# Kernel optimization log

Measured on AMD Instinct MI355X. Metric: run time of the kernel, lower is better.

The kernel has to match this reference:

```python
import jax, jax.numpy as jnp
import numpy as np

H = 16  # num_heads


def setup_inputs() -> dict:
    key = jax.random.key(0)
    ks = jax.random.split(key, 7)
    S, HID, D = 8192, 1280, 80
    n_chunks = 8
    x = jax.random.normal(ks[0], (S, HID), dtype=jnp.float32)
    cos = jax.random.uniform(ks[1], (S, D), dtype=jnp.float32)
    sin = jax.random.uniform(ks[2], (S, D), dtype=jnp.float32)
    Wqkv = jax.random.normal(ks[3], (HID, 3 * HID), dtype=jnp.float32) * (HID ** -0.5)
    bqkv = jnp.zeros((3 * HID,), dtype=jnp.float32)
    Wproj = jax.random.normal(ks[4], (HID, HID), dtype=jnp.float32) * (HID ** -0.5)
    bproj = jnp.zeros((HID,), dtype=jnp.float32)
    cu_seqlens = (jnp.arange(n_chunks + 1, dtype=jnp.int32) * (S // n_chunks))
    return {"x": x, "cos": cos, "sin": sin, "Wqkv": Wqkv, "bqkv": bqkv,
            "Wproj": Wproj, "bproj": bproj, "cu_seqlens": cu_seqlens}


def _apply_rotary(t, cos, sin):
    # t: (S, H, D); cos/sin: (S, D)
    d2 = t.shape[-1] // 2
    x1, x2 = t[..., :d2], t[..., d2:]
    rotated = jnp.concatenate([-x2, x1], axis=-1)
    return t * cos[:, None, :] + rotated * sin[:, None, :]


def reference(x, cos, sin, Wqkv, bqkv, Wproj, bproj, cu_seqlens):
    S, HID = x.shape
    D = HID // H
    inv_scale = 1.0 / np.sqrt(D)
    qkv = (x @ Wqkv + bqkv).reshape(S, 3, H, D)
    q, k, v = qkv[:, 0], qkv[:, 1], qkv[:, 2]  # each (S, H, D)
    q = _apply_rotary(q, cos, sin)
    k = _apply_rotary(k, cos, sin)
    # Equal-size windows: reshape to (n_chunks, L, H, D) -> block-diagonal attention.
    C = cu_seqlens.shape[0] - 1
    L = S // C
    qc = q.reshape(C, L, H, D)
    kc = k.reshape(C, L, H, D)
    vc = v.reshape(C, L, H, D)
    scores = jnp.einsum('cihd,cjhd->chij', qc, kc) * inv_scale
    probs = jax.nn.softmax(scores.astype(jnp.float32), axis=-1).astype(x.dtype)
    out = jnp.einsum('chij,cjhd->cihd', probs, vc)  # (C, L, H, D)
    out = out.reshape(S, HID)
    return out @ Wproj + bproj
```

## Files before the change

### kernel.cpp

```cpp
#include <hip/hip_runtime.h>
#include <math.h>
#include <stdint.h>

#define S_LEN 8192
#define HID   1280
#define NH    16
#define HD    80
#define LCH   1024
#define NCH   8

typedef __attribute__((ext_vector_type(8))) short bf16x8;
typedef __attribute__((ext_vector_type(4))) float f32x4;

__device__ __forceinline__ uint16_t f2bf(float f) {
    union { float f; uint32_t u; } v; v.f = f;
    uint32_t r = v.u + 0x7FFF + ((v.u >> 16) & 1);
    return (uint16_t)(r >> 16);
}
__device__ __forceinline__ float bf2f(uint16_t h) {
    union { uint32_t u; float f; } v; v.u = ((uint32_t)h) << 16;
    return v.f;
}
__device__ __forceinline__ uint16_t f2bf_trunc(float f) {
    union { float f; uint32_t u; } v; v.f = f;
    return (uint16_t)(v.u >> 16);
}

__device__ __forceinline__ void glds16(const void* g, void* l) {
    __builtin_amdgcn_global_load_lds(
        (const __attribute__((address_space(1))) uint32_t*)g,
        (__attribute__((address_space(3))) uint32_t*)l,
        16, 0, 0);
}

#define MFMA16(a, b, c) __builtin_amdgcn_mfma_f32_16x16x32_bf16(a, b, c, 0, 0, 0)
#define SB()  __builtin_amdgcn_sched_barrier(0)
#define BAR() __builtin_amdgcn_s_barrier()

template<int N> __device__ __forceinline__ void vmwait() {
    if constexpr (N == 0) asm volatile("s_waitcnt vmcnt(0)" ::: "memory");
    else if constexpr (N == 2) asm volatile("s_waitcnt vmcnt(2)" ::: "memory");
    else if constexpr (N == 3) asm volatile("s_waitcnt vmcnt(3)" ::: "memory");
    else if constexpr (N == 4) asm volatile("s_waitcnt vmcnt(4)" ::: "memory");
}

__device__ __forceinline__ void stage_tile(const char* gsrc, char* dst, int w,
                                           int kt, int nbytes)
{
    const char* sp = gsrc + (size_t)kt * 64;
    int off = w * 1024;
    glds16(sp + (size_t)off * 40, dst + off);
    off += 8192;
    if (off < nbytes) glds16(sp + (size_t)off * 40, dst + off);
}

__global__ __launch_bounds__(256)
void xsplit_kernel(const float* __restrict__ x, uint16_t* __restrict__ xh,
                   uint16_t* __restrict__ xl)
{
    int idx = (blockIdx.x * 256 + threadIdx.x) * 4;
    float4 v = *(const float4*)(x + idx);
    ushort4 hi, lo;
    hi.x = f2bf(v.x); lo.x = f2bf(v.x - bf2f(hi.x));
    hi.y = f2bf(v.y); lo.y = f2bf(v.y - bf2f(hi.y));
    hi.z = f2bf(v.z); lo.z = f2bf(v.z - bf2f(hi.z));
    hi.w = f2bf(v.w); lo.w = f2bf(v.w - bf2f(hi.w));
    *(ushort4*)(xh + idx) = hi;
    *(ushort4*)(xl + idx) = lo;
}

template<int ND>
__global__ __launch_bounds__(256)
void wsplit_kernel(const float* __restrict__ W, uint16_t* __restrict__ Wth,
                   uint16_t* __restrict__ Wtl)
{
    __shared__ float t[32][33];
    const int tid = threadIdx.x;
    const int n0 = blockIdx.x * 32;
    const int k0 = blockIdx.y * 32;
    for (int i = tid; i < 1024; i += 256) {
        int r = i >> 5, c = i & 31;
        t[r][c] = W[(size_t)(k0 + r) * ND + n0 + c];
    }
    __syncthreads();
    for (int i = tid; i < 1024; i += 256) {
        int r = i >> 5, c = i & 31;
        float f = t[c][r];
        uint16_t hi = f2bf(f);
        size_t o = (size_t)(n0 + r) * HID + k0 + c;
        Wth[o] = hi;
        Wtl[o] = f2bf(f - bf2f(hi));
    }
}

template<int ND, int BN, int NWN, int EPI, int W2, int W3>
__global__ __launch_bounds__(512, 2)
void gemm8p(const uint16_t* __restrict__ Ahp, const uint16_t* __restrict__ Alp,
            const uint16_t* __restrict__ Bth, const uint16_t* __restrict__ Btl,
            const float* __restrict__ bias, float* __restrict__ oF,
            uint16_t* __restrict__ oq, uint16_t* __restrict__ ok,
            uint16_t* __restrict__ ov)
{
    constexpr int NWM = 8 / NWN;
    constexpr int MI  = 256 / (NWM * 16);
    constexpr int NI  = BN / (NWN * 16);
    constexpr int ABYTES = 256 * 64;
    constexpr int BBYTES = BN * 64;
    constexpr int NT = HID / 32;
    static_assert(BN % (NWN * 16) == 0, "tile split");

    __shared__ __align__(1024) uint16_t AsH[2][ABYTES / 2];
    __shared__ __align__(1024) uint16_t AsL[2][ABYTES / 2];
    __shared__ __align__(1024) uint16_t BsH[2][BBYTES / 2];
    __shared__ __align__(1024) uint16_t BsL[2][BBYTES / 2];

    const int tid  = threadIdx.x;
    const int w    = tid >> 6;
    const int lane = tid & 63;
    const int quad = lane >> 4;
    const int l16  = lane & 15;
    const int wm   = w / NWN;
    const int wn   = w % NWN;

    const int n0 = blockIdx.x * BN;
    const int m0 = blockIdx.y * 256;

    const size_t stg = (size_t)(lane >> 2) * (HID * 2)
                     + (size_t)(((lane & 3) ^ ((lane >> 3) & 3)) << 4);
    const char* gAh = (const char*)Ahp + (size_t)m0 * (HID * 2) + stg;
    const char* gAl = (const char*)Alp + (size_t)m0 * (HID * 2) + stg;
    const char* gBh = (const char*)Bth + (size_t)n0 * (HID * 2) + stg;
    const char* gBl = (const char*)Btl + (size_t)n0 * (HID * 2) + stg;

    const int swz  = (quad ^ ((l16 >> 1) & 3)) << 4;
    const int aoff = (wm * (MI * 16) + l16) * 64 + swz;
    const int boff = (wn * (NI * 16) + l16) * 64 + swz;

    f32x4 acc[MI][NI];
    #pragma unroll
    for (int mi = 0; mi < MI; ++mi)
        #pragma unroll
        for (int ni = 0; ni < NI; ++ni) acc[mi][ni] = (f32x4){0.f, 0.f, 0.f, 0.f};

    stage_tile(gAh, (char*)AsH[0], w, 0, ABYTES);
    stage_tile(gBh, (char*)BsH[0], w, 0, BBYTES);
    stage_tile(gBl, (char*)BsL[0], w, 0, BBYTES);
    stage_tile(gAl, (char*)AsL[0], w, 0, ABYTES);
    SB(); vmwait<W3>(); BAR(); SB();

    for (int kt = 0; kt < NT - 1; ++kt) {
        const int s = kt & 1, t = s ^ 1;
        bf16x8 ah[MI], bh[NI];

        #pragma unroll
        for (int mi = 0; mi < MI; ++mi)
            ah[mi] = *(const bf16x8*)((const char*)AsH[s] + aoff + mi * 1024);
        #pragma unroll
        for (int ni = 0; ni < NI; ++ni)
            bh[ni] = *(const bf16x8*)((const char*)BsH[s] + boff + ni * 1024);
        stage_tile(gAh, (char*)AsH[t], w, kt + 1, ABYTES);
        SB(); vmwait<4>(); BAR(); SB();
        __builtin_amdgcn_s_setprio(1);
        #pragma unroll
        for (int mi = 0; mi < MI; ++mi)
            #pragma unroll
            for (int ni = 0; ni < NI; ++ni)
                acc[mi][ni] = MFMA16(ah[mi], bh[ni], acc[mi][ni]);
        __builtin_amdgcn_s_setprio(0);

        bf16x8 bl[NI];
        #pragma unroll
        for (int ni = 0; ni < NI; ++ni)
            bl[ni] = *(const bf16x8*)((const char*)BsL[s] + boff + ni * 1024);
        stage_tile(gBh, (char*)BsH[t], w, kt + 1, BBYTES);
        SB(); vmwait<W2>(); BAR(); SB();
        __builtin_amdgcn_s_setprio(1);
        #pragma unroll
        for (int mi = 0; mi < MI; ++mi)
            #pragma unroll
            for (int ni = 0; ni < NI; ++ni)
                acc[mi][ni] = MFMA16(ah[mi], bl[ni], acc[mi][ni]);
        __builtin_amdgcn_s_setprio(0);

        bf16x8 al[MI];
        #pragma unroll
        for (int mi = 0; mi < MI; ++mi)
            al[mi] = *(const bf16x8*)((const char*)AsL[s] + aoff + mi * 1024);
        stage_tile(gBl, (char*)BsL[t], w, kt + 1, BBYTES);
        stage_tile(gAl, (char*)AsL[t], w, kt + 1, ABYTES);
        SB(); vmwait<W3>(); BAR(); SB();
        __builtin_amdgcn_s_setprio(1);
        #pragma unroll
        for (int mi = 0; mi < MI; ++mi)
            #pragma unroll
            for (int ni = 0; ni < NI; ++ni)
                acc[mi][ni] = MFMA16(al[mi], bh[ni], acc[mi][ni]);
        __builtin_amdgcn_s_setprio(0);
    }

    {
        const int s = (NT - 1) & 1;
        bf16x8 ah[MI], bh[NI];
        #pragma unroll
        for (int mi = 0; mi < MI; ++mi)
            ah[mi] = *(const bf16x8*)((const char*)AsH[s] + aoff + mi * 1024);
        #pragma unroll
        for (int ni = 0; ni < NI; ++ni)
            bh[ni] = *(const bf16x8*)((const char*)BsH[s] + boff + ni * 1024);
        SB(); vmwait<2>(); BAR(); SB();
        __builtin_amdgcn_s_setprio(1);
        #pragma unroll
        for (int mi = 0; mi < MI; ++mi)
            #pragma unroll
            for (int ni = 0; ni < NI; ++ni)
                acc[mi][ni] = MFMA16(ah[mi], bh[ni], acc[mi][ni]);
        __builtin_amdgcn_s_setprio(0);

        bf16x8 bl[NI];
        #pragma unroll
        for (int ni = 0; ni < NI; ++ni)
            bl[ni] = *(const bf16x8*)((const char*)BsL[s] + boff + ni * 1024);
        SB(); vmwait<0>(); BAR(); SB();
        __builtin_amdgcn_s_setprio(1);
        #pragma unroll
        for (int mi = 0; mi < MI; ++mi)
            #pragma unroll
            for (int ni = 0; ni < NI; ++ni)
                acc[mi][ni] = MFMA16(ah[mi], bl[ni], acc[mi][ni]);
        __builtin_amdgcn_s_setprio(0);

        bf16x8 al[MI];
        #pragma unroll
        for (int mi = 0; mi < MI; ++mi)
            al[mi] = *(const bf16x8*)((const char*)AsL[s] + aoff + mi * 1024);
        #pragma unroll
        for (int mi = 0; mi < MI; ++mi)
            #pragma unroll
            for (int ni = 0; ni < NI; ++ni)
                acc[mi][ni] = MFMA16(al[mi], bh[ni], acc[mi][ni]);
    }

    #pragma unroll
    for (int ni = 0; ni < NI; ++ni) {
        const int n = n0 + wn * (NI * 16) + ni * 16 + l16;
        const float bv = bias[n];
        if constexpr (EPI) {
            const int tq  = n / HID;
            const int rem = n - tq * HID;
            const int h   = rem / HD;
            const int d   = rem - h * HD;
            #pragma unroll
            for (int mi = 0; mi < MI; ++mi) {
                const int mb = m0 + wm * (MI * 16) + mi * 16 + quad * 4;
                if (tq == 2) {
                    ushort4 pv;
                    pv.x = f2bf(acc[mi][ni][0] + bv);
                    pv.y = f2bf(acc[mi][ni][1] + bv);
                    pv.z = f2bf(acc[mi][ni][2] + bv);
                    pv.w = f2bf(acc[mi][ni][3] + bv);
                    *(ushort4*)&ov[((size_t)h * HD + d) * S_LEN + mb] = pv;
                } else {
                    uint16_t* dst = (tq == 0) ? oq : ok;
                    #pragma unroll
                    for (int r = 0; r < 4; ++r)
                        dst[((size_t)h * S_LEN + (mb + r)) * HD + d] =
                            f2bf(acc[mi][ni][r] + bv);
                }
            }
        } else {
            #pragma unroll
            for (int mi = 0; mi < MI; ++mi) {
                const int mb = m0 + wm * (MI * 16) + mi * 16 + quad * 4;
                #pragma unroll
                for (int r = 0; r < 4; ++r)
                    oF[(size_t)(mb + r) * ND + n] = acc[mi][ni][r] + bv;
            }
        }
    }
}

__global__ __launch_bounds__(256)
void rope_kernel(uint16_t* __restrict__ qb, uint16_t* __restrict__ kb,
                 const float* __restrict__ cosb, const float* __restrict__ sinb)
{
    int idx = blockIdx.x * 256 + threadIdx.x;
    int d = idx % 40;
    int t = idx / 40;
    int s = t % S_LEN;
    int h = t / S_LEN;
    size_t base = ((size_t)h * S_LEN + s) * HD;
    float c1 = cosb[s * HD + d],      s1 = sinb[s * HD + d];
    float c2 = cosb[s * HD + d + 40], s2 = sinb[s * HD + d + 40];
    float q1 = bf2f(qb[base + d]), q2 = bf2f(qb[base + d + 40]);
    qb[base + d]      = f2bf(q1 * c1 - q2 * s1);
    qb[base + d + 40] = f2bf(q2 * c2 + q1 * s2);
    float k1 = bf2f(kb[base + d]), k2 = bf2f(kb[base + d + 40]);
    kb[base + d]      = f2bf(k1 * c1 - k2 * s1);
    kb[base + d + 40] = f2bf(k2 * c2 + k1 * s2);
}

#define BQ 128
#define BK 64

__global__ __launch_bounds__(256)
void attn_kernel(const uint16_t* __restrict__ qb, const uint16_t* __restrict__ kb,
                 const uint16_t* __restrict__ vt,
                 uint16_t* __restrict__ abh, uint16_t* __restrict__ abl)
{
    __shared__ __align__(16) uint16_t smemA[BQ * HD];
    __shared__ __align__(16) uint16_t ksm[2][BK * HD];
    __shared__ __align__(16) uint16_t vsm[HD * BK];

    const int tid  = threadIdx.x;
    const int w    = tid >> 6;
    const int lane = tid & 63;
    const int quad = lane >> 4;
    const int l16  = lane & 15;

    const int qt = blockIdx.x;
    const int h  = blockIdx.y;
    const int c  = blockIdx.z;
    const int q0 = c * LCH + qt * BQ;

    uint16_t (*psw)[68] = (uint16_t(*)[68])smemA + w * 32;

    {
        const char* qg = (const char*)(qb + ((size_t)h * S_LEN + q0) * HD);
        for (int off = w * 1024; off < BQ * HD * 2; off += 4096)
            glds16(qg + off + lane * 16, (char*)smemA + off);
    }
    __syncthreads();

    bf16x8 qfr[2][3];
    #pragma unroll
    for (int mi = 0; mi < 2; ++mi) {
        const int row = w * 32 + mi * 16 + l16;
        qfr[mi][0] = *(const bf16x8*)&smemA[row * HD + quad * 8];
        qfr[mi][1] = *(const bf16x8*)&smemA[row * HD + 32 + quad * 8];
        bf16x8 z = {0, 0, 0, 0, 0, 0, 0, 0};
        qfr[mi][2] = (quad < 2) ? *(const bf16x8*)&smemA[row * HD + 64 + quad * 8] : z;
    }

    bf16x8 vf5;
    {
        short o = (l16 == 0) ? (short)0x3F80 : (short)0;
        vf5 = (bf16x8){o, o, o, o, o, o, o, o};
    }

    f32x4 Oacc[2][6];
    #pragma unroll
    for (int mi = 0; mi < 2; ++mi)
        #pragma unroll
        for (int d = 0; d < 6; d++) Oacc[mi][d] = (f32x4){0.f, 0.f, 0.f, 0.f};

    const float C2 = 0.11180339887498949f * 1.4426950408889634f;
    const char* kg0 = (const char*)(kb + ((size_t)h * S_LEN + c * LCH) * HD);
    const size_t vrow_stride = (size_t)S_LEN * 2;
    const char* vg0 = (const char*)vt + (size_t)h * HD * S_LEN * 2 + (size_t)(c * LCH) * 2;

    {
        const char* kg = kg0;
        for (int off = w * 1024; off < BK * HD * 2; off += 4096)
            glds16(kg + off + lane * 16, (char*)&ksm[0][0] + off);
    }

    for (int kt = 0; kt < LCH / BK; ++kt) {
        __syncthreads();

        {
            const char* vg = vg0 + (size_t)(kt * BK) * 2;
            for (int off = w * 1024; off < HD * BK * 2; off += 4096) {
                int o   = off + lane * 16;
                int row = o >> 7;
                int col = o & 127;
                glds16(vg + (size_t)row * vrow_stride + col, (char*)vsm + off);
            }
        }

        const uint16_t* ksb = &ksm[kt & 1][0];
        f32x4 sc[2][4];
        #pragma unroll
        for (int mi = 0; mi < 2; ++mi)
            #pragma unroll
            for (int ns = 0; ns < 4; ns++) sc[mi][ns] = (f32x4){0.f, 0.f, 0.f, 0.f};
        #pragma unroll
        for (int ns = 0; ns < 4; ++ns) {
            const int kr = ns * 16 + l16;
            bf16x8 kf0 = *(const bf16x8*)&ksb[kr * HD + quad * 8];
            bf16x8 kf1 = *(const bf16x8*)&ksb[kr * HD + 32 + quad * 8];
            bf16x8 z = {0, 0, 0, 0, 0, 0, 0, 0};
            bf16x8 kf2 = (quad < 2) ? *(const bf16x8*)&ksb[kr * HD + 64 + quad * 8] : z;
            #pragma unroll
            for (int mi = 0; mi < 2; ++mi) {
                sc[mi][ns] = MFMA16(qfr[mi][0], kf0, sc[mi][ns]);
                sc[mi][ns] = MFMA16(qfr[mi][1], kf1, sc[mi][ns]);
                sc[mi][ns] = MFMA16(qfr[mi][2], kf2, sc[mi][ns]);
            }
        }

        #pragma unroll
        for (int mi = 0; mi < 2; ++mi)
            #pragma unroll
            for (int r = 0; r < 4; ++r) {
                const int prow = mi * 16 + quad * 4 + r;
                #pragma unroll
                for (int ns = 0; ns < 4; ++ns)
                    psw[prow][ns * 16 + l16] =
                        f2bf_trunc(exp2f(sc[mi][ns][r] * C2));
            }

        __syncthreads();

        if (kt + 1 < LCH / BK) {
            const char* kg = kg0 + (size_t)(kt + 1) * BK * HD * 2;
            char* dst = (char*)&ksm[(kt + 1) & 1][0];
            for (int off = w * 1024; off < BK * HD * 2; off += 4096)
                glds16(kg + off + lane * 16, dst + off);
        }

        #pragma unroll
        for (int kc = 0; kc < 2; ++kc) {
            bf16x8 pf[2];
            #pragma unroll
            for (int mi = 0; mi < 2; ++mi) {
                const uint16_t* pp = &psw[mi * 16 + l16][kc * 32 + quad * 8];
                ((uint2*)&pf[mi])[0] = *(const uint2*)(pp);
                ((uint2*)&pf[mi])[1] = *(const uint2*)(pp + 4);
            }
            #pragma unroll
            for (int ds = 0; ds < 5; ++ds) {
                bf16x8 vf = *(const bf16x8*)&vsm[(ds * 16 + l16) * BK + kc * 32 + quad * 8];
                #pragma unroll
                for (int mi = 0; mi < 2; ++mi)
                    Oacc[mi][ds] = MFMA16(pf[mi], vf, Oacc[mi][ds]);
            }
            #pragma unroll
            for (int mi = 0; mi < 2; ++mi)
                Oacc[mi][5] = MFMA16(pf[mi], vf5, Oacc[mi][5]);
        }
    }

    #pragma unroll
    for (int mi = 0; mi < 2; ++mi)
        #pragma unroll
        for (int r = 0; r < 4; ++r) {
            float l = __shfl(Oacc[mi][5][r], lane & 48);
            float inv = 1.f / l;
            const int srow = q0 + w * 32 + mi * 16 + quad * 4 + r;
            const size_t rowbase = (size_t)srow * HID + h * HD;
            #pragma unroll
            for (int ds = 0; ds < 5; ++ds) {
                float f = Oacc[mi][ds][r] * inv;
                uint16_t hi = f2bf(f);
                abh[rowbase + ds * 16 + l16] = hi;
                abl[rowbase + ds * 16 + l16] = f2bf(f - bf2f(hi));
            }
        }
}

extern "C" void kernel_launch(void* const* d_in, const int* in_sizes, int n_in,
                              void* d_out, int out_size, void* d_ws, size_t ws_size,
                              hipStream_t stream)
{
    const float* x     = (const float*)d_in[0];
    const float* cosb  = (const float*)d_in[1];
    const float* sinb  = (const float*)d_in[2];
    const float* Wqkv  = (const float*)d_in[3];
    const float* bqkv  = (const float*)d_in[4];
    const float* Wproj = (const float*)d_in[5];
    const float* bproj = (const float*)d_in[6];
    float* out = (float*)d_out;

    const size_t E = (size_t)NH * S_LEN * HD;
    uint16_t* qb  = (uint16_t*)d_ws;
    uint16_t* kb  = qb + E;
    uint16_t* vt  = kb + E;
    uint16_t* xh  = vt + E;
    uint16_t* xl  = xh + E;
    uint16_t* wth = xl + E;
    uint16_t* wtl = wth + (size_t)3 * HID * HID;

    xsplit_kernel<<<(S_LEN * HID) / (256 * 4), 256, 0, stream>>>(x, xh, xl);
    wsplit_kernel<3 * HID><<<dim3(3 * HID / 32, HID / 32), 256, 0, stream>>>(Wqkv, wth, wtl);
    gemm8p<3 * HID, 256, 4, 1, 4, 4>
        <<<dim3(3 * HID / 256, S_LEN / 256), 512, 0, stream>>>(
        xh, xl, wth, wtl, bqkv, nullptr, qb, kb, vt);
    rope_kernel<<<(S_LEN * NH * 40) / 256, 256, 0, stream>>>(qb, kb, cosb, sinb);
    attn_kernel<<<dim3(LCH / BQ, NH, NCH), 256, 0, stream>>>(qb, kb, vt, xh, xl);
    wsplit_kernel<HID><<<dim3(HID / 32, HID / 32), 256, 0, stream>>>(Wproj, wth, wtl);
    gemm8p<HID, 160, 2, 0, 3, 3>
        <<<dim3(HID / 160, S_LEN / 256), 512, 0, stream>>>(
        xh, xl, wth, wtl, bproj, out, nullptr, nullptr, nullptr);
}
```

Measured before the change: 504.7 us.

## Regroup GEMM prefetch stages, double attention query tile, fuse exp into score loop

The split-bf16 GEMM main loop now issues all next-tile loads in two groups and waits on them at two points instead of three, with one barrier left without a vmcnt wait. The attention kernel moves to 512 threads with a 256-row query block, and load strides are adjusted to match. Scores are now computed with K as the A operand, so each lane holds transposed results that are exponentiated and packed straight into the P buffer as pairs. This cuts register pressure and the scattered scalar LDS stores. The risks are hazards from the changed wait and barrier placement in the GEMM, and occupancy or LDS limits from the larger attention block.

```diff
diff --git a/kernel.cpp b/kernel.cpp
--- a/kernel.cpp
+++ b/kernel.cpp
@@ -21,9 +21,9 @@
     union { uint32_t u; float f; } v; v.u = ((uint32_t)h) << 16;
     return v.f;
 }
-__device__ __forceinline__ uint16_t f2bf_trunc(float f) {
-    union { float f; uint32_t u; } v; v.f = f;
-    return (uint16_t)(v.u >> 16);
+__device__ __forceinline__ uint32_t pk2(float a, float b) {
+    union { float f; uint32_t u; } x, y; x.f = a; y.f = b;
+    return (x.u >> 16) | (y.u & 0xFFFF0000u);
 }
 
 __device__ __forceinline__ void glds16(const void* g, void* l) {
@@ -39,7 +39,6 @@
 
 template<int N> __device__ __forceinline__ void vmwait() {
     if constexpr (N == 0) asm volatile("s_waitcnt vmcnt(0)" ::: "memory");
-    else if constexpr (N == 2) asm volatile("s_waitcnt vmcnt(2)" ::: "memory");
     else if constexpr (N == 3) asm volatile("s_waitcnt vmcnt(3)" ::: "memory");
     else if constexpr (N == 4) asm volatile("s_waitcnt vmcnt(4)" ::: "memory");
 }
@@ -93,7 +92,7 @@
     }
 }
 
-template<int ND, int BN, int NWN, int EPI, int W2, int W3>
+template<int ND, int BN, int NWN, int EPI, int W1>
 __global__ __launch_bounds__(512, 2)
 void gemm8p(const uint16_t* __restrict__ Ahp, const uint16_t* __restrict__ Alp,
             const uint16_t* __restrict__ Bth, const uint16_t* __restrict__ Btl,
@@ -146,7 +145,7 @@
     stage_tile(gBh, (char*)BsH[0], w, 0, BBYTES);
     stage_tile(gBl, (char*)BsL[0], w, 0, BBYTES);
     stage_tile(gAl, (char*)AsL[0], w, 0, ABYTES);
-    SB(); vmwait<W3>(); BAR(); SB();
+    SB(); vmwait<W1>(); BAR(); SB();
 
     for (int kt = 0; kt < NT - 1; ++kt) {
         const int s = kt & 1, t = s ^ 1;
@@ -159,7 +158,8 @@
         for (int ni = 0; ni < NI; ++ni)
             bh[ni] = *(const bf16x8*)((const char*)BsH[s] + boff + ni * 1024);
         stage_tile(gAh, (char*)AsH[t], w, kt + 1, ABYTES);
-        SB(); vmwait<4>(); BAR(); SB();
+        stage_tile(gBh, (char*)BsH[t], w, kt + 1, BBYTES);
+        SB(); vmwait<W1>(); BAR(); SB();
         __builtin_amdgcn_s_setprio(1);
         #pragma unroll
         for (int mi = 0; mi < MI; ++mi)
@@ -172,8 +172,9 @@
         #pragma unroll
         for (int ni = 0; ni < NI; ++ni)
             bl[ni] = *(const bf16x8*)((const char*)BsL[s] + boff + ni * 1024);
-        stage_tile(gBh, (char*)BsH[t], w, kt + 1, BBYTES);
-        SB(); vmwait<W2>(); BAR(); SB();
+        stage_tile(gBl, (char*)BsL[t], w, kt + 1, BBYTES);
+        stage_tile(gAl, (char*)AsL[t], w, kt + 1, ABYTES);
+        SB(); BAR(); SB();
         __builtin_amdgcn_s_setprio(1);
         #pragma unroll
         for (int mi = 0; mi < MI; ++mi)
@@ -186,9 +187,7 @@
         #pragma unroll
         for (int mi = 0; mi < MI; ++mi)
             al[mi] = *(const bf16x8*)((const char*)AsL[s] + aoff + mi * 1024);
-        stage_tile(gBl, (char*)BsL[t], w, kt + 1, BBYTES);
-        stage_tile(gAl, (char*)AsL[t], w, kt + 1, ABYTES);
-        SB(); vmwait<W3>(); BAR(); SB();
+        SB(); vmwait<W1>(); BAR(); SB();
         __builtin_amdgcn_s_setprio(1);
         #pragma unroll
         for (int mi = 0; mi < MI; ++mi)
@@ -207,7 +206,7 @@
         #pragma unroll
         for (int ni = 0; ni < NI; ++ni)
             bh[ni] = *(const bf16x8*)((const char*)BsH[s] + boff + ni * 1024);
-        SB(); vmwait<2>(); BAR(); SB();
+        SB(); vmwait<0>(); BAR(); SB();
         __builtin_amdgcn_s_setprio(1);
         #pragma unroll
         for (int mi = 0; mi < MI; ++mi)
@@ -220,14 +219,11 @@
         #pragma unroll
         for (int ni = 0; ni < NI; ++ni)
             bl[ni] = *(const bf16x8*)((const char*)BsL[s] + boff + ni * 1024);
-        SB(); vmwait<0>(); BAR(); SB();
-        __builtin_amdgcn_s_setprio(1);
         #pragma unroll
         for (int mi = 0; mi < MI; ++mi)
             #pragma unroll
             for (int ni = 0; ni < NI; ++ni)
                 acc[mi][ni] = MFMA16(ah[mi], bl[ni], acc[mi][ni]);
-        __builtin_amdgcn_s_setprio(0);
 
         bf16x8 al[MI];
         #pragma unroll
@@ -299,10 +295,10 @@
     kb[base + d + 40] = f2bf(k2 * c2 + k1 * s2);
 }
 
-#define BQ 128
+#define BQ 256
 #define BK 64
 
-__global__ __launch_bounds__(256)
+__global__ __launch_bounds__(512, 4)
 void attn_kernel(const uint16_t* __restrict__ qb, const uint16_t* __restrict__ kb,
                  const uint16_t* __restrict__ vt,
                  uint16_t* __restrict__ abh, uint16_t* __restrict__ abl)
@@ -326,7 +322,7 @@
 
     {
         const char* qg = (const char*)(qb + ((size_t)h * S_LEN + q0) * HD);
-        for (int off = w * 1024; off < BQ * HD * 2; off += 4096)
+        for (int off = w * 1024; off < BQ * HD * 2; off += 8192)
             glds16(qg + off + lane * 16, (char*)smemA + off);
     }
     __syncthreads();
@@ -360,7 +356,7 @@
 
     {
         const char* kg = kg0;
-        for (int off = w * 1024; off < BK * HD * 2; off += 4096)
+        for (int off = w * 1024; off < BK * HD * 2; off += 8192)
             glds16(kg + off + lane * 16, (char*)&ksm[0][0] + off);
     }
 
@@ -369,7 +365,7 @@
 
         {
             const char* vg = vg0 + (size_t)(kt * BK) * 2;
-            for (int off = w * 1024; off < HD * BK * 2; off += 4096) {
+            for (int off = w * 1024; off < HD * BK * 2; off += 8192) {
                 int o   = off + lane * 16;
                 int row = o >> 7;
                 int col = o & 127;
@@ -378,11 +374,6 @@
         }
 
         const uint16_t* ksb = &ksm[kt & 1][0];
-        f32x4 sc[2][4];
-        #pragma unroll
-        for (int mi = 0; mi < 2; ++mi)
-            #pragma unroll
-            for (int ns = 0; ns < 4; ns++) sc[mi][ns] = (f32x4){0.f, 0.f, 0.f, 0.f};
         #pragma unroll
         for (int ns = 0; ns < 4; ++ns) {
             const int kr = ns * 16 + l16;
@@ -392,29 +383,25 @@
             bf16x8 kf2 = (quad < 2) ? *(const bf16x8*)&ksb[kr * HD + 64 + quad * 8] : z;
             #pragma unroll
             for (int mi = 0; mi < 2; ++mi) {
-                sc[mi][ns] = MFMA16(qfr[mi][0], kf0, sc[mi][ns]);
-                sc[mi][ns] = MFMA16(qfr[mi][1], kf1, sc[mi][ns]);
-                sc[mi][ns] = MFMA16(qfr[mi][2], kf2, sc[mi][ns]);
-            }
-        }
-
-        #pragma unroll
-        for (int mi = 0; mi < 2; ++mi)
-            #pragma unroll
-            for (int r = 0; r < 4; ++r) {
-                const int prow = mi * 16 + quad * 4 + r;
-                #pragma unroll
-                for (int ns = 0; ns < 4; ++ns)
-                    psw[prow][ns * 16 + l16] =
-                        f2bf_trunc(exp2f(sc[mi][ns][r] * C2));
-            }
+                f32x4 s = (f32x4){0.f, 0.f, 0.f, 0.f};
+                s = MFMA16(kf0, qfr[mi][0], s);
+                s = MFMA16(kf1, qfr[mi][1], s);
+                s = MFMA16(kf2, qfr[mi][2], s);
+                float e0 = exp2f(s[0] * C2);
+                float e1 = exp2f(s[1] * C2);
+                float e2 = exp2f(s[2] * C2);
+                float e3 = exp2f(s[3] * C2);
+                *(uint2*)&psw[mi * 16 + l16][ns * 16 + quad * 4] =
+                    (uint2){pk2(e0, e1), pk2(e2, e3)};
+            }
+        }
 
         __syncthreads();
 
         if (kt + 1 < LCH / BK) {
             const char* kg = kg0 + (size_t)(kt + 1) * BK * HD * 2;
             char* dst = (char*)&ksm[(kt + 1) & 1][0];
-            for (int off = w * 1024; off < BK * HD * 2; off += 4096)
+            for (int off = w * 1024; off < BK * HD * 2; off += 8192)
                 glds16(kg + off + lane * 16, dst + off);
         }
 
@@ -482,13 +469,13 @@
 
     xsplit_kernel<<<(S_LEN * HID) / (256 * 4), 256, 0, stream>>>(x, xh, xl);
     wsplit_kernel<3 * HID><<<dim3(3 * HID / 32, HID / 32), 256, 0, stream>>>(Wqkv, wth, wtl);
-    gemm8p<3 * HID, 256, 4, 1, 4, 4>
+    gemm8p<3 * HID, 256, 4, 1, 4>
         <<<dim3(3 * HID / 256, S_LEN / 256), 512, 0, stream>>>(
         xh, xl, wth, wtl, bqkv, nullptr, qb, kb, vt);
     rope_kernel<<<(S_LEN * NH * 40) / 256, 256, 0, stream>>>(qb, kb, cosb, sinb);
-    attn_kernel<<<dim3(LCH / BQ, NH, NCH), 256, 0, stream>>>(qb, kb, vt, xh, xl);
+    attn_kernel<<<dim3(LCH / BQ, NH, NCH), 512, 0, stream>>>(qb, kb, vt, xh, xl);
     wsplit_kernel<HID><<<dim3(HID / 32, HID / 32), 256, 0, stream>>>(Wproj, wth, wtl);
-    gemm8p<HID, 160, 2, 0, 3, 3>
+    gemm8p<HID, 160, 2, 0, 3>
         <<<dim3(HID / 160, S_LEN / 256), 512, 0, stream>>>(
         xh, xl, wth, wtl, bproj, out, nullptr, nullptr, nullptr);
 }
```

Result: faster. 488.4 us (-3.2%).
